# Kernel tuning notes

Measured on AMD Instinct MI355X. Metric: run time of the kernel, lower is better.

Reference implementation:

```python
import jax, jax.numpy as jnp
import numpy as np

B = 2048   # windows per stream
N = 49     # tokens per 7x7 window
C = 192    # dim
H = 6      # heads
D = C // H # head_dim = 32
WH = WW = 7
SCALE = D ** -0.5


def _rel_pos_index():
    coords = np.stack(np.meshgrid(np.arange(WH), np.arange(WW), indexing='ij')).reshape(2, -1)
    rc = (coords[:, :, None] - coords[:, None, :]).transpose(1, 2, 0)  # [N,N,2]
    rc[..., 0] += WH - 1
    rc[..., 1] += WW - 1
    rc[..., 0] *= 2 * WW - 1
    return rc.sum(-1)  # [N,N] ints in [0, 169)

RPI = _rel_pos_index()


def setup_inputs() -> dict:
    key = jax.random.key(0)
    ks = jax.random.split(key, 16)
    w = lambda k, sh: jax.random.normal(k, sh, jnp.float32) * 0.02
    s = lambda v: jnp.asarray(v, jnp.float32)
    return {
        'x_sa': jax.random.normal(ks[0], (2 * B, N, C), jnp.float32),
        'x_ca': jax.random.normal(ks[1], (B, 2 * N, C), jnp.float32),
        'lambda_sa': s(0.1),
        'lambda_ca': s(0.1),
        'sa_enh': s(0.1),
        'ca_enh': s(0.1),
        'W_sa_qkv': w(ks[2], (C, 3 * C)), 'b_sa_qkv': jnp.zeros((3 * C,), jnp.float32),
        'W_sa_ct': w(ks[3], (C, C)), 'W_sa_cr': w(ks[4], (C, C)),
        'W_ca_q': w(ks[5], (C, C)), 'b_ca_q': jnp.zeros((C,), jnp.float32),
        'W_ca_kv': w(ks[6], (C, 2 * C)), 'b_ca_kv': jnp.zeros((2 * C,), jnp.float32),
        'W_ca_ct': w(ks[7], (C, C)), 'W_ca_cr': w(ks[8], (C, C)),
        'rpb_table': w(ks[9], ((2 * WH - 1) * (2 * WW - 1), H)),
        'W_proj_sa': w(ks[10], (C, C)), 'b_proj_sa': jnp.zeros((C,), jnp.float32),
        'W_proj_ca': w(ks[11], (C, C)), 'b_proj_ca': jnp.zeros((C,), jnp.float32),
    }


def _heads(x):  # [B,N,C] -> [B,H,N,D]
    b, n, _ = x.shape
    return x.reshape(b, n, H, D).transpose(0, 2, 1, 3)


def _merge(x):  # [B,H,N,D] -> [B,N,C]
    b = x.shape[0]
    return x.transpose(0, 2, 1, 3).reshape(b, -1, C)


def _diff_attn(qt, kt, vt, qr, kr, vr, bias, lam_param):
    at = jax.nn.softmax(jnp.einsum('bhnd,bhmd->bhnm', qt * SCALE, kt) + bias, axis=-1)
    ar = jax.nn.softmax(jnp.einsum('bhnd,bhmd->bhnm', qr * SCALE, kr) + bias, axis=-1)
    lam = jnp.clip(jax.nn.sigmoid(lam_param), 0.01, 0.99)
    ot = jnp.einsum('bhnm,bhmd->bhnd', at - lam * ar, vt)
    orf = jnp.einsum('bhnm,bhmd->bhnd', ar - lam * at, vr)
    return ot, orf


def _forward(x_sa, x_ca, lambda_sa, lambda_ca, sa_enh, ca_enh,
             W_sa_qkv, b_sa_qkv, W_sa_ct, W_sa_cr,
             W_ca_q, b_ca_q, W_ca_kv, b_ca_kv, W_ca_ct, W_ca_cr,
             rpb_table, W_proj_sa, b_proj_sa, W_proj_ca, b_proj_ca):
    bias = rpb_table[RPI.reshape(-1)].reshape(N, N, H).transpose(2, 0, 1)  # [H,N,N]

    # ---- self-attention path (streams concat on batch) ----
    xt, xr = x_sa[:B], x_sa[B:]
    te = xt + sa_enh * (xr @ W_sa_cr)
    re = xr + sa_enh * (xt @ W_sa_ct)
    qkv_t = (te @ W_sa_qkv + b_sa_qkv).reshape(B, N, 3, H, D).transpose(2, 0, 3, 1, 4)
    qkv_r = (re @ W_sa_qkv + b_sa_qkv).reshape(B, N, 3, H, D).transpose(2, 0, 3, 1, 4)
    ot, orf = _diff_attn(qkv_t[0], qkv_t[1], qkv_t[2], qkv_r[0], qkv_r[1], qkv_r[2], bias, lambda_sa)
    out_sa = jnp.concatenate([_merge(ot) @ W_proj_sa + b_proj_sa,
                              _merge(orf) @ W_proj_sa + b_proj_sa], axis=0)  # [2B,N,C]

    # ---- cross-attention path (streams concat on sequence) ----
    xt, xr = x_ca[:, :N, :], x_ca[:, N:, :]
    te = xt + ca_enh * (xr @ W_ca_cr)
    re = xr + ca_enh * (xt @ W_ca_ct)
    qt = _heads(te @ W_ca_q + b_ca_q)
    qr = _heads(re @ W_ca_q + b_ca_q)
    xcat = jnp.concatenate([te, re], axis=1)  # [B,2N,C]
    kv = (xcat @ W_ca_kv + b_ca_kv).reshape(B, 2 * N, 2, H, D).transpose(2, 0, 3, 1, 4)
    k, v = kv[0], kv[1]  # [B,H,2N,D]
    ot, orf = _diff_attn(qt, k[:, :, :N], v[:, :, :N], qr, k[:, :, N:], v[:, :, N:], bias, lambda_ca)
    out_ca = jnp.concatenate([_merge(ot) @ W_proj_ca + b_proj_ca,
                              _merge(orf) @ W_proj_ca + b_proj_ca], axis=1)  # [B,2N,C]

    return jnp.stack([out_sa, out_ca.reshape(2 * B, N, C)], axis=0)  # [2,2B,N,C]


def reference(x_sa, x_ca, lambda_sa, lambda_ca, sa_enh, ca_enh,
              W_sa_qkv, b_sa_qkv, W_sa_ct, W_sa_cr,
              W_ca_q, b_ca_q, W_ca_kv, b_ca_kv, W_ca_ct, W_ca_cr,
              rpb_table, W_proj_sa, b_proj_sa, W_proj_ca, b_proj_ca):
    return _forward(x_sa, x_ca, lambda_sa, lambda_ca, sa_enh, ca_enh,
                    W_sa_qkv, b_sa_qkv, W_sa_ct, W_sa_cr,
                    W_ca_q, b_ca_q, W_ca_kv, b_ca_kv, W_ca_ct, W_ca_cr,
                    rpb_table, W_proj_sa, b_proj_sa, W_proj_ca, b_proj_ca)
```

## Files before the change

kernel.cpp:

```cpp
#include <hip/hip_runtime.h>
#include <cmath>

static constexpr float SCALE_ = 0.17677669529663687f;

typedef __attribute__((ext_vector_type(8))) _Float16 f16x8;
typedef __attribute__((ext_vector_type(8))) ushort u16x8;
typedef __attribute__((ext_vector_type(4))) float f32x4;

__device__ inline ushort f16u(float f) {
    union { _Float16 h; ushort u; } c;
    c.h = (_Float16)f;
    return c.u;
}

__device__ __forceinline__ void gld16(const ushort* g, ushort* l) {
    __builtin_amdgcn_global_load_lds(
        (const __attribute__((address_space(1))) unsigned int*)g,
        (__attribute__((address_space(3))) unsigned int*)l,
        16, 0, 0);
}

struct SmallmmJobs {
    const float* Wa[6];
    const float* Wb[6];
    const float* sc[6];
    float*       out[6];
    int          NCb[6];
    int          base[7];
};
__global__ __launch_bounds__(256) void smallmm_all(SmallmmJobs J)
{
    int b = blockIdx.x;
    int j = 0;
    #pragma unroll
    for (int k = 1; k < 6; ++k) if (b >= J.base[k]) j = k;
    int idx = (b - J.base[j]) * 256 + threadIdx.x;
    int NCb = J.NCb[j];
    int n4  = NCb >> 2;
    int m   = idx / n4;
    int n0  = (idx - m * n4) << 2;
    if (m >= 192) return;
    const float* Wa = J.Wa[j];
    const float* Wb = J.Wb[j];
    float s = J.sc[j][0];
    float ax = 0.f, ay = 0.f, az = 0.f, aw = 0.f;
    for (int k = 0; k < 192; ++k) {
        float a = Wa[m * 192 + k];
        const float4 bv = *(const float4*)(Wb + (size_t)k * NCb + n0);
        ax += a * bv.x; ay += a * bv.y; az += a * bv.z; aw += a * bv.w;
    }
    float4 r = make_float4(ax * s, ay * s, az * s, aw * s);
    *(float4*)(J.out[j] + (size_t)m * NCb + n0) = r;
}

struct WtJobs {
    const float* W[11];
    ushort*      dh[11];
    int          NC[11];
    int          dNC[11];
    int          coff[11];
    int          base[12];
};
__global__ __launch_bounds__(256) void conv_wT_all(WtJobs J)
{
    int b = blockIdx.x;
    int j = 0;
    #pragma unroll
    for (int k = 1; k < 11; ++k) if (b >= J.base[k]) j = k;
    int idx = (b - J.base[j]) * 256 + threadIdx.x;
    int NC = J.NC[j];
    if (idx >= NC * 192) return;
    int n = idx / 192, k = idx - n * 192;
    float f = J.W[j][(long long)k * NC + n];
    long long o = ((long long)(k >> 5) * J.dNC[j] + J.coff[j] + n) * 32 + (k & 31);
    J.dh[j][o] = f16u(f);
}

__global__ __launch_bounds__(256) void concat_bias(
    const float* __restrict__ a, const float* __restrict__ b,
    float* __restrict__ d)
{
    int i = blockIdx.x * 256 + threadIdx.x;
    if (i < 192) d[i] = a[i];
    else if (i < 576) d[i] = b[i - 192];
}

__global__ __launch_bounds__(256) void conv_x2(
    const float* __restrict__ src_t, const float* __restrict__ src_r,
    long long src_bs,
    ushort* __restrict__ dh_t, ushort* __restrict__ dh_r, int Mc)
{
    const long long SS = (long long)Mc * 32;
    const long long total8 = (long long)Mc * 24;
    for (long long t = (long long)blockIdx.x * 256 + threadIdx.x; t < 2 * total8;
         t += (long long)gridDim.x * 256) {
        const int second = (t >= total8);
        long long ti = second ? t - total8 : t;
        const float* src = second ? src_r : src_t;
        ushort* dh = second ? dh_r : dh_t;
        int m  = (int)(ti / 24);
        int c8 = (int)(ti - (long long)m * 24) * 8;
        int bb = m / 49, r = m - bb * 49;
        const float* sp = src + (long long)bb * src_bs + r * 192 + c8;
        float4 v0 = *(const float4*)sp;
        float4 v1 = *(const float4*)(sp + 4);
        float f[8] = {v0.x, v0.y, v0.z, v0.w, v1.x, v1.y, v1.z, v1.w};
        u16x8 h8;
        #pragma unroll
        for (int e = 0; e < 8; ++e) h8[e] = f16u(f[e]);
        long long o = (long long)(c8 >> 5) * SS + (long long)m * 32 + (c8 & 31);
        *(u16x8*)(dh + o) = h8;
    }
}

template<int NC, bool DUAL, bool F32OUT>
__global__ __launch_bounds__(256, 5) void gemm_f16(
    const ushort* __restrict__ A1a, const ushort* __restrict__ A2a,
    const ushort* __restrict__ B2a, ushort* __restrict__ outHa,
    float* __restrict__ outFa,
    const ushort* __restrict__ A1b, const ushort* __restrict__ A2b,
    const ushort* __restrict__ B2b, ushort* __restrict__ outHb,
    float* __restrict__ outFb,
    const ushort* __restrict__ B1, const float* __restrict__ bias,
    long long out_bs, int M)
{
    __shared__ __align__(16) ushort AHs[2][2048];
    __shared__ __align__(16) ushort BHs[2][6144];

    constexpr int GX = NC / 192;
    const int nwg = gridDim.x;
    const int orig = blockIdx.x;
    const int q8 = nwg >> 3, r8b = nwg & 7;
    const int xc = orig & 7, ix = orig >> 3;
    const int L = (xc < r8b ? xc * (q8 + 1) : r8b * (q8 + 1) + (xc - r8b) * q8) + ix;
    const int bm = L / (GX * 2);
    const int rem = L - bm * (GX * 2);
    const int bn = rem % GX;
    const int z  = rem / GX;

    const ushort* Ah1 = z ? A1b : A1a;
    const ushort* Ah2 = z ? A2b : A2a;
    const ushort* Bh2 = z ? B2b : B2a;

    const int tid = threadIdx.x;
    const int lane = tid & 63, wv = tid >> 6;
    const int wm = (wv >> 1) * 32;
    const int wn = (wv & 1) * 96;
    const int lr = lane & 15, lg = lane >> 4;
    const long long SS = (long long)M * 32;
    constexpr int NP = DUAL ? 6 : 3;

    const int at_row = tid >> 2;
    const int at_c   = (tid & 3) ^ ((tid >> 3) & 3);
    const long long a_src = (long long)(bm * 64 + at_row) * 32 + at_c * 8;
    int b_src[3];
    #pragma unroll
    for (int k = 0; k < 3; ++k) {
        int t = k * 256 + tid;
        int row = t >> 2, c = (t & 3) ^ ((t >> 3) & 3);
        b_src[k] = (bn * 192 + row) * 32 + c * 8;
    }
    const int wdst = wv * 512;

    int aoff[2], boff[6];
    #pragma unroll
    for (int i = 0; i < 2; ++i) {
        int row = wm + 16 * i + lr;
        aoff[i] = (row * 4 + (lg ^ ((row >> 1) & 3))) * 8;
    }
    #pragma unroll
    for (int j = 0; j < 6; ++j) {
        int row = wn + 16 * j + lr;
        boff[j] = (row * 4 + (lg ^ ((row >> 1) & 3))) * 8;
    }

    f32x4 acc[2][6] = {};

    #pragma unroll
    for (int p = 0; p < NP; ++p) {
        #pragma unroll
        for (int hbf = 0; hbf < 2; ++hbf) {
            const int s = 2 * p + hbf;
            const int k6 = (s < 6) ? s : s - 6;
            const ushort* AHp = (!DUAL || s < 6) ? Ah1 : Ah2;
            const ushort* BHp = (!DUAL || s < 6) ? B1  : Bh2;
            const long long asb = (long long)k6 * SS;
            const int bsb = k6 * (NC * 32);
            gld16(AHp + asb + a_src, AHs[hbf] + wdst);
            #pragma unroll
            for (int k = 0; k < 3; ++k)
                gld16(BHp + bsb + b_src[k], BHs[hbf] + k * 2048 + wdst);
        }
        __syncthreads();

        #pragma unroll
        for (int hbf = 0; hbf < 2; ++hbf) {
            f16x8 ah[2];
            #pragma unroll
            for (int i = 0; i < 2; ++i)
                ah[i] = *(const f16x8*)&AHs[hbf][aoff[i]];
            #pragma unroll
            for (int j = 0; j < 6; ++j) {
                f16x8 bh = *(const f16x8*)&BHs[hbf][boff[j]];
                #pragma unroll
                for (int i = 0; i < 2; ++i)
                    acc[i][j] = __builtin_amdgcn_mfma_f32_16x16x32_f16(ah[i], bh, acc[i][j], 0, 0, 0);
            }
        }
        __syncthreads();
    }

    #pragma unroll
    for (int j = 0; j < 6; ++j) {
        const int c = bn * 192 + wn + 16 * j + lr;
        const float bv = bias ? bias[c] : 0.f;
        #pragma unroll
        for (int i = 0; i < 2; ++i)
            #pragma unroll
            for (int r = 0; r < 4; ++r) {
                int m = bm * 64 + wm + 16 * i + 4 * lg + r;
                if (m < M) {
                    float f = acc[i][j][r] + bv;
                    if constexpr (F32OUT) {
                        float* outF = z ? outFb : outFa;
                        int b2 = m / 49, r2 = m - b2 * 49;
                        outF[(long long)b2 * out_bs + r2 * 192 + c] = f;
                    } else {
                        ushort* outH = z ? outHb : outHa;
                        long long o = (long long)(c >> 5) * SS + (long long)m * 32 + (c & 31);
                        outH[o] = f16u(f);
                    }
                }
            }
    }
}

__global__ __launch_bounds__(256, 4) void attn_f16(
    const ushort* __restrict__ qT, const ushort* __restrict__ kT,
    const ushort* __restrict__ vT,
    const ushort* __restrict__ qR, const ushort* __restrict__ kR,
    const ushort* __restrict__ vR,
    long long SS,
    const float* __restrict__ rpb, const float* __restrict__ lam_ptr,
    ushort* __restrict__ otH, ushort* __restrict__ orH)
{
    __shared__ __align__(16) ushort Pth[64][72];
    __shared__ __align__(16) ushort Vs[2][32][70];
    __shared__ float bias_s[169];

    const int tid = threadIdx.x;
    const int bb = blockIdx.x / 6;
    const int h  = blockIdx.x - bb * 6;
    const int lane = tid & 63;
    const int w  = tid >> 6;
    const int li = lane & 15;
    const int lg = lane >> 4;
    const long long rowbase = (long long)bb * 49 * 32;
    const long long hb = (long long)h * SS + rowbase;

    for (int idx = tid; idx < 169; idx += 256) bias_s[idx] = rpb[idx * 6 + h];

    {
        const ushort* vsrc[2] = {vT + hb, vR + hb};
        for (int c = tid; c < 392; c += 256) {
            int s  = c / 196;
            int r2 = c - s * 196;
            int j  = r2 >> 2;
            int d4 = (r2 & 3) * 8;
            u16x8 v = *(const u16x8*)(vsrc[s] + j * 32 + d4);
            #pragma unroll
            for (int e = 0; e < 8; ++e) Vs[s][d4 + e][j] = v[e];
        }
        for (int c = tid; c < 2 * 32 * 21; c += 256) {
            int s  = c / (32 * 21);
            int r1 = c - s * (32 * 21);
            int d  = r1 / 21;
            int j  = 49 + (r1 - d * 21);
            Vs[s][d][j] = 0;
        }
    }

    float lraw = lam_ptr[0];
    float lam = 1.f / (1.f + __expf(-lraw));
    lam = fminf(fmaxf(lam, 0.01f), 0.99f);

    const int irow = min(w * 16 + li, 48);

    f32x4 st[2][4];
    #pragma unroll
    for (int s = 0; s < 2; ++s) {
        const ushort* qb = (s ? qR : qT) + hb;
        const ushort* kb = (s ? kR : kT) + hb;
        f16x8 qh = *(const f16x8*)(qb + irow * 32 + 8 * lg);
        #pragma unroll
        for (int jt = 0; jt < 4; ++jt) {
            int jr = jt * 16 + li; if (jr > 48) jr = 48;
            f16x8 kh = *(const f16x8*)(kb + jr * 32 + 8 * lg);
            f32x4 c = {};
            c = __builtin_amdgcn_mfma_f32_16x16x32_f16(kh, qh, c, 0, 0, 0);
            st[s][jt] = c;
        }
    }
    __syncthreads();

    const int ri = (irow * 9363) >> 16;
    const int ci = irow - 7 * ri;
    float bias_v[4][4];
    #pragma unroll
    for (int jt = 0; jt < 4; ++jt)
        #pragma unroll
        for (int r = 0; r < 4; ++r) {
            int j = jt * 16 + 4 * lg + r;
            int jc = (j < 49) ? j : 48;
            int rj = (jc * 9363) >> 16;
            int cj = jc - 7 * rj;
            bias_v[jt][r] = bias_s[(ri - rj + 6) * 13 + (ci - cj + 6)];
        }

    float p[2][4][4];
    #pragma unroll
    for (int s = 0; s < 2; ++s) {
        float m = -1e30f;
        #pragma unroll
        for (int jt = 0; jt < 4; ++jt)
            #pragma unroll
            for (int r = 0; r < 4; ++r) {
                int j = jt * 16 + 4 * lg + r;
                float sv = (j < 49) ? (st[s][jt][r] * SCALE_ + bias_v[jt][r]) : -1e30f;
                p[s][jt][r] = sv;
                m = fmaxf(m, sv);
            }
        m = fmaxf(m, __shfl_xor(m, 16));
        m = fmaxf(m, __shfl_xor(m, 32));
        float sum = 0.f;
        #pragma unroll
        for (int jt = 0; jt < 4; ++jt)
            #pragma unroll
            for (int r = 0; r < 4; ++r) {
                float e = __expf(p[s][jt][r] - m);
                p[s][jt][r] = e;
                sum += e;
            }
        sum += __shfl_xor(sum, 16);
        sum += __shfl_xor(sum, 32);
        float inv = 1.f / sum;
        #pragma unroll
        for (int jt = 0; jt < 4; ++jt)
            #pragma unroll
            for (int r = 0; r < 4; ++r)
                p[s][jt][r] *= inv;
    }

    const int prow = w * 16 + li;
    #pragma unroll
    for (int s = 0; s < 2; ++s) {
        #pragma unroll
        for (int jt = 0; jt < 4; ++jt) {
            ushort4 h4;
            #pragma unroll
            for (int r = 0; r < 4; ++r) {
                float at = p[0][jt][r], ar = p[1][jt][r];
                float f = (s == 0) ? (at - lam * ar) : (ar - lam * at);
                ((ushort*)&h4)[r] = f16u(f);
            }
            *(ushort4*)&Pth[prow][jt * 16 + 4 * lg] = h4;
        }

        f32x4 acc[2] = {};
        #pragma unroll
        for (int ks = 0; ks < 2; ++ks) {
            f16x8 pa = *(const f16x8*)&Pth[prow][ks * 32 + 8 * lg];
            #pragma unroll
            for (int dt = 0; dt < 2; ++dt) {
                f16x8 vh = *(const f16x8*)&Vs[s][dt * 16 + li][ks * 32 + 8 * lg];
                acc[dt] = __builtin_amdgcn_mfma_f32_16x16x32_f16(pa, vh, acc[dt], 0, 0, 0);
            }
        }
        ushort* oph = s ? orH : otH;
        #pragma unroll
        for (int dt = 0; dt < 2; ++dt)
            #pragma unroll
            for (int r = 0; r < 4; ++r) {
                int i = w * 16 + 4 * lg + r;
                if (i < 49) {
                    long long o = (long long)h * SS + rowbase + (long long)i * 32 + dt * 16 + li;
                    oph[o] = f16u(acc[dt][r]);
                }
            }
    }
}

extern "C" void kernel_launch(void* const* d_in, const int* in_sizes, int n_in,
                              void* d_out, int out_size, void* d_ws, size_t ws_size,
                              hipStream_t stream)
{
    const float* x_sa      = (const float*)d_in[0];
    const float* x_ca      = (const float*)d_in[1];
    const float* lam_sa    = (const float*)d_in[2];
    const float* lam_ca    = (const float*)d_in[3];
    const float* sa_enh    = (const float*)d_in[4];
    const float* ca_enh    = (const float*)d_in[5];
    const float* W_sa_qkv  = (const float*)d_in[6];
    const float* b_sa_qkv  = (const float*)d_in[7];
    const float* W_sa_ct   = (const float*)d_in[8];
    const float* W_sa_cr   = (const float*)d_in[9];
    const float* W_ca_q    = (const float*)d_in[10];
    const float* b_ca_q    = (const float*)d_in[11];
    const float* W_ca_kv   = (const float*)d_in[12];
    const float* b_ca_kv   = (const float*)d_in[13];
    const float* W_ca_ct   = (const float*)d_in[14];
    const float* W_ca_cr   = (const float*)d_in[15];
    const float* rpb       = (const float*)d_in[16];
    const float* W_proj_sa = (const float*)d_in[17];
    const float* b_proj_sa = (const float*)d_in[18];
    const float* W_proj_ca = (const float*)d_in[19];
    const float* b_proj_ca = (const float*)d_in[20];
    float* out = (float*)d_out;
    float* ws  = (float*)d_ws;

    float* CW0 = ws;
    float* CW1 = CW0 + 110592;
    float* CW2 = CW1 + 110592;
    float* CW3 = CW2 + 36864;
    float* CW4 = CW3 + 36864;
    float* CW5 = CW4 + 73728;
    float* bqkv_ca = CW5 + 73728;

    {
        SmallmmJobs J;
        J.Wa[0]=W_sa_cr; J.Wb[0]=W_sa_qkv; J.sc[0]=sa_enh; J.out[0]=CW0; J.NCb[0]=576;
        J.Wa[1]=W_sa_ct; J.Wb[1]=W_sa_qkv; J.sc[1]=sa_enh; J.out[1]=CW1; J.NCb[1]=576;
        J.Wa[2]=W_ca_cr; J.Wb[2]=W_ca_q;   J.sc[2]=ca_enh; J.out[2]=CW2; J.NCb[2]=192;
        J.Wa[3]=W_ca_ct; J.Wb[3]=W_ca_q;   J.sc[3]=ca_enh; J.out[3]=CW3; J.NCb[3]=192;
        J.Wa[4]=W_ca_cr; J.Wb[4]=W_ca_kv;  J.sc[4]=ca_enh; J.out[4]=CW4; J.NCb[4]=384;
        J.Wa[5]=W_ca_ct; J.Wb[5]=W_ca_kv;  J.sc[5]=ca_enh; J.out[5]=CW5; J.NCb[5]=384;
        int bs[7] = {0,108,216,252,288,360,432};
        for (int i = 0; i < 7; ++i) J.base[i] = bs[i];
        smallmm_all<<<432, 256, 0, stream>>>(J);
    }
    concat_bias<<<3, 256, 0, stream>>>(b_ca_q, b_ca_kv, bqkv_ca);

    ushort* wb = (ushort*)(ws + 442944);
    ushort* WsaqH  = wb;
    ushort* C0H    = WsaqH + 110592;
    ushort* C1H    = C0H + 110592;
    ushort* WcqkvH = C1H + 110592;
    ushort* C24H   = WcqkvH + 110592;
    ushort* C35H   = C24H + 110592;
    ushort* WpsH   = C35H + 110592;
    ushort* WpcH   = WpsH + 36864;
    ushort* chunkU = WpcH + 36864;

    {
        WtJobs J;
        const float* Ws[11] = {W_sa_qkv, CW0, CW1,
                               W_ca_q, CW2, CW3,
                               W_ca_kv, CW4, CW5,
                               W_proj_sa, W_proj_ca};
        ushort* Ds[11] = {WsaqH, C0H, C1H,
                          WcqkvH, C24H, C35H,
                          WcqkvH, C24H, C35H,
                          WpsH, WpcH};
        int NCs[11]  = {576,576,576, 192,192,192, 384,384,384, 192,192};
        int dNCs[11] = {576,576,576, 576,576,576, 576,576,576, 192,192};
        int coffs[11]= {0,0,0, 0,0,0, 192,192,192, 0,0};
        int bs[12] = {0,432,864,1296,1440,1584,1728,2016,2304,2592,2736,2880};
        for (int i = 0; i < 11; ++i) {
            J.W[i]=Ws[i]; J.dh[i]=Ds[i]; J.NC[i]=NCs[i];
            J.dNC[i]=dNCs[i]; J.coff[i]=coffs[i];
        }
        for (int i = 0; i < 12; ++i) J.base[i] = bs[i];
        conv_wT_all<<<2880, 256, 0, stream>>>(J);
    }

    long long avail = (long long)ws_size - 442944LL * 4 - 737280LL * 2 - 65536;
    int cbmax = (int)(avail / 188160);
    if (cbmax > 1024) cbmax = 1024;
    if (cbmax < 1) cbmax = 1;

    const long long OUT1 = 2LL * 2048 * 49 * 192;
    dim3 blk(256);

    for (int c0 = 0; c0 < 2048; c0 += cbmax) {
        int cb = (c0 + cbmax <= 2048) ? cbmax : (2048 - c0);
        int M = cb * 49;
        long long SS = (long long)M * 32;
        int gy = (M + 63) / 64;
        int cblk = (int)(((long long)M * 48 + 255) / 256);
        if (cblk > 4096) cblk = 4096;

        dim3 g1(6 * gy), g2(2 * gy);

        ushort* XtH = chunkU;
        ushort* XrH = XtH + (long long)cbmax * 9408;
        ushort* QtH = XrH + (long long)cbmax * 9408;
        ushort* QrH = QtH + (long long)cbmax * 28224;
        ushort* OtH = QrH + (long long)cbmax * 28224;
        ushort* OrH = OtH + (long long)cbmax * 9408;

        conv_x2<<<cblk, blk, 0, stream>>>(
            x_sa + (long long)c0 * 9408, x_sa + (2048LL + c0) * 9408, 9408,
            XtH, XrH, M);

        gemm_f16<576, true, false><<<g1, blk, 0, stream>>>(
            XtH, XrH, C0H, QtH, nullptr,
            XrH, XtH, C1H, QrH, nullptr,
            WsaqH, b_sa_qkv, 0, M);

        attn_f16<<<cb * 6, blk, 0, stream>>>(
            QtH, QtH + 6 * SS, QtH + 12 * SS,
            QrH, QrH + 6 * SS, QrH + 12 * SS,
            SS, rpb, lam_sa, OtH, OrH);

        gemm_f16<192, false, true><<<g2, blk, 0, stream>>>(
            OtH, nullptr, nullptr, nullptr, out + (long long)c0 * 9408,
            OrH, nullptr, nullptr, nullptr, out + (2048LL + c0) * 9408,
            WpsH, b_proj_sa, 9408, M);

        ushort* CXtH = chunkU;
        ushort* CXrH = CXtH + (long long)cbmax * 9408;
        ushort* CQtH = CXrH + (long long)cbmax * 9408;
        ushort* CQrH = CQtH + (long long)cbmax * 28224;
        ushort* COtH = CQrH + (long long)cbmax * 28224;
        ushort* COrH = COtH + (long long)cbmax * 9408;

        conv_x2<<<cblk, blk, 0, stream>>>(
            x_ca + (long long)c0 * 18816, x_ca + (long long)c0 * 18816 + 9408, 18816,
            CXtH, CXrH, M);

        gemm_f16<576, true, false><<<g1, blk, 0, stream>>>(
            CXtH, CXrH, C24H, CQtH, nullptr,
            CXrH, CXtH, C35H, CQrH, nullptr,
            WcqkvH, bqkv_ca, 0, M);

        attn_f16<<<cb * 6, blk, 0, stream>>>(
            CQtH, CQtH + 6 * SS, CQtH + 12 * SS,
            CQrH, CQrH + 6 * SS, CQrH + 12 * SS,
            SS, rpb, lam_ca, COtH, COrH);

        gemm_f16<192, false, true><<<g2, blk, 0, stream>>>(
            COtH, nullptr, nullptr, nullptr, out + OUT1 + (long long)c0 * 18816,
            COrH, nullptr, nullptr, nullptr, out + OUT1 + (long long)c0 * 18816 + 9408,
            WpcH, b_proj_ca, 18816, M);
    }
}
```

Measured before the change: 747.0 us.

## Batch self- and cross-attention streams into shared multi-job kernel launches

Merges the self-attention and cross-attention pipelines so each stage (convert, QKV GEMM, attention, projection GEMM) runs as one launch covering both streams, selected through per-job pointer tables. This halves the launch count and doubles grid size per launch, which improves occupancy and tail behaviour. Attention outputs now reuse the converted-input buffers. The per-chunk workspace divisor grows, so chunks may shrink when the workspace is small.

```diff
diff --git a/kernel.cpp b/kernel.cpp
--- a/kernel.cpp
+++ b/kernel.cpp
@@ -85,19 +85,22 @@
     else if (i < 576) d[i] = b[i - 192];
 }
 
-__global__ __launch_bounds__(256) void conv_x2(
-    const float* __restrict__ src_t, const float* __restrict__ src_r,
-    long long src_bs,
-    ushort* __restrict__ dh_t, ushort* __restrict__ dh_r, int Mc)
+struct ConvJobs {
+    const float* src[4];
+    ushort*      dst[4];
+    long long    bs[4];
+};
+__global__ __launch_bounds__(256) void conv_x4(ConvJobs J, int Mc)
 {
     const long long SS = (long long)Mc * 32;
-    const long long total8 = (long long)Mc * 24;
-    for (long long t = (long long)blockIdx.x * 256 + threadIdx.x; t < 2 * total8;
+    const long long per = (long long)Mc * 24;
+    for (long long t = (long long)blockIdx.x * 256 + threadIdx.x; t < 4 * per;
          t += (long long)gridDim.x * 256) {
-        const int second = (t >= total8);
-        long long ti = second ? t - total8 : t;
-        const float* src = second ? src_r : src_t;
-        ushort* dh = second ? dh_r : dh_t;
+        int j = (int)(t / per);
+        long long ti = t - (long long)j * per;
+        const float* src = J.src[j];
+        ushort* dh = J.dst[j];
+        long long src_bs = J.bs[j];
         int m  = (int)(ti / 24);
         int c8 = (int)(ti - (long long)m * 24) * 8;
         int bb = m / 49, r = m - bb * 49;
@@ -113,16 +116,18 @@
     }
 }
 
-template<int NC, bool DUAL, bool F32OUT>
-__global__ __launch_bounds__(256, 5) void gemm_f16(
-    const ushort* __restrict__ A1a, const ushort* __restrict__ A2a,
-    const ushort* __restrict__ B2a, ushort* __restrict__ outHa,
-    float* __restrict__ outFa,
-    const ushort* __restrict__ A1b, const ushort* __restrict__ A2b,
-    const ushort* __restrict__ B2b, ushort* __restrict__ outHb,
-    float* __restrict__ outFb,
-    const ushort* __restrict__ B1, const float* __restrict__ bias,
-    long long out_bs, int M)
+struct GemmJobs {
+    const ushort* A1[4];
+    const ushort* A2[4];
+    const ushort* B1[4];
+    const ushort* B2[4];
+    ushort*       outH[4];
+    float*        outF[4];
+    const float*  bias[4];
+    long long     out_bs[4];
+};
+template<int NC, bool DUAL, bool F32OUT, int NJ>
+__global__ __launch_bounds__(256, 5) void gemm_f16(GemmJobs G, int M)
 {
     __shared__ __align__(16) ushort AHs[2][2048];
     __shared__ __align__(16) ushort BHs[2][6144];
@@ -133,14 +138,15 @@
     const int q8 = nwg >> 3, r8b = nwg & 7;
     const int xc = orig & 7, ix = orig >> 3;
     const int L = (xc < r8b ? xc * (q8 + 1) : r8b * (q8 + 1) + (xc - r8b) * q8) + ix;
-    const int bm = L / (GX * 2);
-    const int rem = L - bm * (GX * 2);
-    const int bn = rem % GX;
-    const int z  = rem / GX;
-
-    const ushort* Ah1 = z ? A1b : A1a;
-    const ushort* Ah2 = z ? A2b : A2a;
-    const ushort* Bh2 = z ? B2b : B2a;
+    const int bm = L / (GX * NJ);
+    const int rem = L - bm * (GX * NJ);
+    const int jj = rem / GX;
+    const int bn = rem - jj * GX;
+
+    const ushort* Ah1 = G.A1[jj];
+    const ushort* Ah2 = G.A2[jj];
+    const ushort* B1p = G.B1[jj];
+    const ushort* Bh2 = G.B2[jj];
 
     const int tid = threadIdx.x;
     const int lane = tid & 63, wv = tid >> 6;
@@ -183,7 +189,7 @@
             const int s = 2 * p + hbf;
             const int k6 = (s < 6) ? s : s - 6;
             const ushort* AHp = (!DUAL || s < 6) ? Ah1 : Ah2;
-            const ushort* BHp = (!DUAL || s < 6) ? B1  : Bh2;
+            const ushort* BHp = (!DUAL || s < 6) ? B1p : Bh2;
             const long long asb = (long long)k6 * SS;
             const int bsb = k6 * (NC * 32);
             gld16(AHp + asb + a_src, AHs[hbf] + wdst);
@@ -213,7 +219,7 @@
     #pragma unroll
     for (int j = 0; j < 6; ++j) {
         const int c = bn * 192 + wn + 16 * j + lr;
-        const float bv = bias ? bias[c] : 0.f;
+        const float bv = G.bias[jj] ? G.bias[jj][c] : 0.f;
         #pragma unroll
         for (int i = 0; i < 2; ++i)
             #pragma unroll
@@ -222,35 +228,36 @@
                 if (m < M) {
                     float f = acc[i][j][r] + bv;
                     if constexpr (F32OUT) {
-                        float* outF = z ? outFb : outFa;
                         int b2 = m / 49, r2 = m - b2 * 49;
-                        outF[(long long)b2 * out_bs + r2 * 192 + c] = f;
+                        G.outF[jj][(long long)b2 * G.out_bs[jj] + r2 * 192 + c] = f;
                     } else {
-                        ushort* outH = z ? outHb : outHa;
                         long long o = (long long)(c >> 5) * SS + (long long)m * 32 + (c & 31);
-                        outH[o] = f16u(f);
+                        G.outH[jj][o] = f16u(f);
                     }
                 }
             }
     }
 }
 
+struct AttnJobs {
+    const ushort* qT[2]; const ushort* kT[2]; const ushort* vT[2];
+    const ushort* qR[2]; const ushort* kR[2]; const ushort* vR[2];
+    const float*  lam[2];
+    ushort* otH[2]; ushort* orH[2];
+};
 __global__ __launch_bounds__(256, 4) void attn_f16(
-    const ushort* __restrict__ qT, const ushort* __restrict__ kT,
-    const ushort* __restrict__ vT,
-    const ushort* __restrict__ qR, const ushort* __restrict__ kR,
-    const ushort* __restrict__ vR,
-    long long SS,
-    const float* __restrict__ rpb, const float* __restrict__ lam_ptr,
-    ushort* __restrict__ otH, ushort* __restrict__ orH)
+    AttnJobs J, long long SS, const float* __restrict__ rpb)
 {
     __shared__ __align__(16) ushort Pth[64][72];
     __shared__ __align__(16) ushort Vs[2][32][70];
     __shared__ float bias_s[169];
 
     const int tid = threadIdx.x;
-    const int bb = blockIdx.x / 6;
-    const int h  = blockIdx.x - bb * 6;
+    const int nb6 = gridDim.x >> 1;
+    const int job = (blockIdx.x >= nb6) ? 1 : 0;
+    const int bidx = blockIdx.x - job * nb6;
+    const int bb = bidx / 6;
+    const int h  = bidx - bb * 6;
     const int lane = tid & 63;
     const int w  = tid >> 6;
     const int li = lane & 15;
@@ -258,10 +265,15 @@
     const long long rowbase = (long long)bb * 49 * 32;
     const long long hb = (long long)h * SS + rowbase;
 
+    const ushort* qTp = J.qT[job]; const ushort* kTp = J.kT[job];
+    const ushort* vTp = J.vT[job];
+    const ushort* qRp = J.qR[job]; const ushort* kRp = J.kR[job];
+    const ushort* vRp = J.vR[job];
+
     for (int idx = tid; idx < 169; idx += 256) bias_s[idx] = rpb[idx * 6 + h];
 
     {
-        const ushort* vsrc[2] = {vT + hb, vR + hb};
+        const ushort* vsrc[2] = {vTp + hb, vRp + hb};
         for (int c = tid; c < 392; c += 256) {
             int s  = c / 196;
             int r2 = c - s * 196;
@@ -280,7 +292,7 @@
         }
     }
 
-    float lraw = lam_ptr[0];
+    float lraw = J.lam[job][0];
     float lam = 1.f / (1.f + __expf(-lraw));
     lam = fminf(fmaxf(lam, 0.01f), 0.99f);
 
@@ -289,8 +301,8 @@
     f32x4 st[2][4];
     #pragma unroll
     for (int s = 0; s < 2; ++s) {
-        const ushort* qb = (s ? qR : qT) + hb;
-        const ushort* kb = (s ? kR : kT) + hb;
+        const ushort* qb = (s ? qRp : qTp) + hb;
+        const ushort* kb = (s ? kRp : kTp) + hb;
         f16x8 qh = *(const f16x8*)(qb + irow * 32 + 8 * lg);
         #pragma unroll
         for (int jt = 0; jt < 4; ++jt) {
@@ -376,7 +388,7 @@
                 acc[dt] = __builtin_amdgcn_mfma_f32_16x16x32_f16(pa, vh, acc[dt], 0, 0, 0);
             }
         }
-        ushort* oph = s ? orH : otH;
+        ushort* oph = s ? J.orH[job] : J.otH[job];
         #pragma unroll
         for (int dt = 0; dt < 2; ++dt)
             #pragma unroll
@@ -474,7 +486,7 @@
     }
 
     long long avail = (long long)ws_size - 442944LL * 4 - 737280LL * 2 - 65536;
-    int cbmax = (int)(avail / 188160);
+    int cbmax = (int)(avail / 301056);
     if (cbmax > 1024) cbmax = 1024;
     if (cbmax < 1) cbmax = 1;
 
@@ -486,61 +498,70 @@
         int M = cb * 49;
         long long SS = (long long)M * 32;
         int gy = (M + 63) / 64;
-        int cblk = (int)(((long long)M * 48 + 255) / 256);
+        int cblk = (int)(((long long)M * 96 + 255) / 256);
         if (cblk > 4096) cblk = 4096;
 
-        dim3 g1(6 * gy), g2(2 * gy);
-
-        ushort* XtH = chunkU;
-        ushort* XrH = XtH + (long long)cbmax * 9408;
-        ushort* QtH = XrH + (long long)cbmax * 9408;
-        ushort* QrH = QtH + (long long)cbmax * 28224;
-        ushort* OtH = QrH + (long long)cbmax * 28224;
-        ushort* OrH = OtH + (long long)cbmax * 9408;
-
-        conv_x2<<<cblk, blk, 0, stream>>>(
-            x_sa + (long long)c0 * 9408, x_sa + (2048LL + c0) * 9408, 9408,
-            XtH, XrH, M);
-
-        gemm_f16<576, true, false><<<g1, blk, 0, stream>>>(
-            XtH, XrH, C0H, QtH, nullptr,
-            XrH, XtH, C1H, QrH, nullptr,
-            WsaqH, b_sa_qkv, 0, M);
-
-        attn_f16<<<cb * 6, blk, 0, stream>>>(
-            QtH, QtH + 6 * SS, QtH + 12 * SS,
-            QrH, QrH + 6 * SS, QrH + 12 * SS,
-            SS, rpb, lam_sa, OtH, OrH);
-
-        gemm_f16<192, false, true><<<g2, blk, 0, stream>>>(
-            OtH, nullptr, nullptr, nullptr, out + (long long)c0 * 9408,
-            OrH, nullptr, nullptr, nullptr, out + (2048LL + c0) * 9408,
-            WpsH, b_proj_sa, 9408, M);
-
-        ushort* CXtH = chunkU;
+        ushort* XtH  = chunkU;
+        ushort* XrH  = XtH  + (long long)cbmax * 9408;
+        ushort* QtH  = XrH  + (long long)cbmax * 9408;
+        ushort* QrH  = QtH  + (long long)cbmax * 28224;
+        ushort* CXtH = QrH  + (long long)cbmax * 28224;
         ushort* CXrH = CXtH + (long long)cbmax * 9408;
         ushort* CQtH = CXrH + (long long)cbmax * 9408;
         ushort* CQrH = CQtH + (long long)cbmax * 28224;
-        ushort* COtH = CQrH + (long long)cbmax * 28224;
-        ushort* COrH = COtH + (long long)cbmax * 9408;
-
-        conv_x2<<<cblk, blk, 0, stream>>>(
-            x_ca + (long long)c0 * 18816, x_ca + (long long)c0 * 18816 + 9408, 18816,
-            CXtH, CXrH, M);
-
-        gemm_f16<576, true, false><<<g1, blk, 0, stream>>>(
-            CXtH, CXrH, C24H, CQtH, nullptr,
-            CXrH, CXtH, C35H, CQrH, nullptr,
-            WcqkvH, bqkv_ca, 0, M);
-
-        attn_f16<<<cb * 6, blk, 0, stream>>>(
-            CQtH, CQtH + 6 * SS, CQtH + 12 * SS,
-            CQrH, CQrH + 6 * SS, CQrH + 12 * SS,
-            SS, rpb, lam_ca, COtH, COrH);
-
-        gemm_f16<192, false, true><<<g2, blk, 0, stream>>>(
-            COtH, nullptr, nullptr, nullptr, out + OUT1 + (long long)c0 * 18816,
-            COrH, nullptr, nullptr, nullptr, out + OUT1 + (long long)c0 * 18816 + 9408,
-            WpcH, b_proj_ca, 18816, M);
-    }
-}
+        ushort* OtH  = XtH;
+        ushort* OrH  = XrH;
+        ushort* COtH = CXtH;
+        ushort* COrH = CXrH;
+
+        {
+            ConvJobs J;
+            J.src[0] = x_sa + (long long)c0 * 9408;           J.dst[0] = XtH;  J.bs[0] = 9408;
+            J.src[1] = x_sa + (2048LL + c0) * 9408;           J.dst[1] = XrH;  J.bs[1] = 9408;
+            J.src[2] = x_ca + (long long)c0 * 18816;          J.dst[2] = CXtH; J.bs[2] = 18816;
+            J.src[3] = x_ca + (long long)c0 * 18816 + 9408;   J.dst[3] = CXrH; J.bs[3] = 18816;
+            conv_x4<<<cblk, blk, 0, stream>>>(J, M);
+        }
+
+        {
+            GemmJobs G;
+            G.A1[0]=XtH;  G.A2[0]=XrH;  G.B1[0]=WsaqH;  G.B2[0]=C0H;
+            G.outH[0]=QtH;  G.outF[0]=nullptr; G.bias[0]=b_sa_qkv; G.out_bs[0]=0;
+            G.A1[1]=XrH;  G.A2[1]=XtH;  G.B1[1]=WsaqH;  G.B2[1]=C1H;
+            G.outH[1]=QrH;  G.outF[1]=nullptr; G.bias[1]=b_sa_qkv; G.out_bs[1]=0;
+            G.A1[2]=CXtH; G.A2[2]=CXrH; G.B1[2]=WcqkvH; G.B2[2]=C24H;
+            G.outH[2]=CQtH; G.outF[2]=nullptr; G.bias[2]=bqkv_ca;  G.out_bs[2]=0;
+            G.A1[3]=CXrH; G.A2[3]=CXtH; G.B1[3]=WcqkvH; G.B2[3]=C35H;
+            G.outH[3]=CQrH; G.outF[3]=nullptr; G.bias[3]=bqkv_ca;  G.out_bs[3]=0;
+            gemm_f16<576, true, false, 4><<<dim3(12 * gy), blk, 0, stream>>>(G, M);
+        }
+
+        {
+            AttnJobs J;
+            J.qT[0]=QtH;           J.kT[0]=QtH + 6 * SS;  J.vT[0]=QtH + 12 * SS;
+            J.qR[0]=QrH;           J.kR[0]=QrH + 6 * SS;  J.vR[0]=QrH + 12 * SS;
+            J.lam[0]=lam_sa;       J.otH[0]=OtH;          J.orH[0]=OrH;
+            J.qT[1]=CQtH;          J.kT[1]=CQtH + 6 * SS; J.vT[1]=CQtH + 12 * SS;
+            J.qR[1]=CQrH;          J.kR[1]=CQrH + 6 * SS; J.vR[1]=CQrH + 12 * SS;
+            J.lam[1]=lam_ca;       J.otH[1]=COtH;         J.orH[1]=COrH;
+            attn_f16<<<2 * cb * 6, blk, 0, stream>>>(J, SS, rpb);
+        }
+
+        {
+            GemmJobs G;
+            G.A1[0]=OtH;  G.A2[0]=nullptr; G.B1[0]=WpsH; G.B2[0]=nullptr;
+            G.outH[0]=nullptr; G.outF[0]=out + (long long)c0 * 9408;
+            G.bias[0]=b_proj_sa; G.out_bs[0]=9408;
+            G.A1[1]=OrH;  G.A2[1]=nullptr; G.B1[1]=WpsH; G.B2[1]=nullptr;
+            G.outH[1]=nullptr; G.outF[1]=out + (2048LL + c0) * 9408;
+            G.bias[1]=b_proj_sa; G.out_bs[1]=9408;
+            G.A1[2]=COtH; G.A2[2]=nullptr; G.B1[2]=WpcH; G.B2[2]=nullptr;
+            G.outH[2]=nullptr; G.outF[2]=out + OUT1 + (long long)c0 * 18816;
+            G.bias[2]=b_proj_ca; G.out_bs[2]=18816;
+            G.A1[3]=COrH; G.A2[3]=nullptr; G.B1[3]=WpcH; G.B2[3]=nullptr;
+            G.outH[3]=nullptr; G.outF[3]=out + OUT1 + (long long)c0 * 18816 + 9408;
+            G.bias[3]=b_proj_ca; G.out_bs[3]=18816;
+            gemm_f16<192, false, true, 4><<<dim3(4 * gy), blk, 0, stream>>>(G, M);
+        }
+    }
+}
```

Result: slower. 787.6 us (+5.4%).
